# Optimization experiments

Measured on AMD Instinct MI355X. Metric: run time of the kernel, lower is better.

The kernel has to match this reference:

```python
import jax, jax.numpy as jnp
import numpy as np

N_ENT = 50000
N_REL = 16
D_E = 64
D_R = 64
D_OUT = 32
N_EDGE = 1000000


def setup_inputs() -> dict:
    key = jax.random.key(0)
    ks = jax.random.split(key, 8)
    # 0.1 scale keeps tanh / softmax in a realistic (non-saturated) range,
    # mimicking trained embedding magnitudes.
    entity_table = jax.random.normal(ks[0], (N_ENT, D_E), dtype=jnp.float32) * 0.1
    relation_table = jax.random.normal(ks[1], (N_REL, D_R), dtype=jnp.float32) * 0.1
    W_R = jax.random.normal(ks[2], (N_REL, D_E, D_R), dtype=jnp.float32) * (1.0 / np.sqrt(D_E))
    W1 = jax.random.normal(ks[3], (D_E, D_OUT), dtype=jnp.float32) * (1.0 / np.sqrt(D_E))
    b1 = jnp.zeros((D_OUT,), dtype=jnp.float32)
    W2 = jax.random.normal(ks[4], (D_E, D_OUT), dtype=jnp.float32) * (1.0 / np.sqrt(D_E))
    b2 = jnp.zeros((D_OUT,), dtype=jnp.float32)
    src = jax.random.randint(ks[5], (N_EDGE,), 0, N_ENT, dtype=jnp.int32)
    dst = jax.random.randint(ks[6], (N_EDGE,), 0, N_ENT, dtype=jnp.int32)
    etype = jax.random.randint(ks[7], (N_EDGE,), 0, N_REL, dtype=jnp.int32)
    return {"entity_table": entity_table, "relation_table": relation_table,
            "W_R": W_R, "W1": W1, "b1": b1, "W2": W2, "b2": b2,
            "src": src, "dst": dst, "etype": etype}


def reference(entity_table, relation_table, W_R, W1, b1, W2, b2, src, dst, etype):
    """KGAT calc_att (per-relation edge attention + edge softmax) followed by
    one bi-interaction Aggregator layer (dropout = identity, eval mode)."""
    n_nodes = entity_table.shape[0]
    # Per-relation projection of all node embeddings (grouped GEMM form of the
    # per-relation loop in compute_attention): [R, N, d_r]
    proj = jnp.einsum('nd,rde->rne', entity_table, W_R)
    r_mul_h = proj[etype, src]            # [E, d_r]  h W_r per edge
    r_mul_t = proj[etype, dst]            # [E, d_r]  t W_r per edge
    r_e = relation_table[etype]           # [E, d_r]
    # att = (h W_r) . tanh(t W_r + r)
    att = jnp.sum(r_mul_h * jnp.tanh(r_mul_t + r_e), axis=-1)  # [E]
    # edge softmax grouped by destination node
    att_max = jax.ops.segment_max(att, dst, num_segments=n_nodes)     # [N]
    ex = jnp.exp(att - att_max[dst])
    denom = jax.ops.segment_sum(ex, dst, num_segments=n_nodes)        # [N]
    a = ex / denom[dst]                                               # [E]
    # u_mul_e + sum: N_h[v] = sum_{(u->v)} a_e * node[u]
    msg = a[:, None] * entity_table[src]                              # [E, d]
    N_h = jax.ops.segment_sum(msg, dst, num_segments=n_nodes)         # [N, d]
    node = entity_table
    # bi-interaction aggregator (LeakyReLU slope 0.01, torch default)
    out1 = jax.nn.leaky_relu((node + N_h) @ W1 + b1)
    out2 = jax.nn.leaky_relu((node * N_h) @ W2 + b2)
    return out1 + out2
```

## Files before the change

kernel.cpp:

```cpp
#include <hip/hip_runtime.h>
#include <math.h>

#define NREL 16
#define DE 64
#define DOUT 32
#define NPART 16
#define TQ 392

typedef __attribute__((ext_vector_type(8))) short bf16x8;
typedef __attribute__((ext_vector_type(16))) float f32x16;
typedef __attribute__((ext_vector_type(2))) float f32x2;

__device__ __forceinline__ short f2bf(float f) {
    unsigned u = __builtin_bit_cast(unsigned, f);
    unsigned r = (u + 0x7FFFu + ((u >> 16) & 1u)) >> 16;
    return (short)r;
}
__device__ __forceinline__ float bf2f(short s) {
    unsigned u = ((unsigned)(unsigned short)s) << 16;
    return __builtin_bit_cast(float, u);
}
__device__ __forceinline__ unsigned char f2fp8(float f) {
    int p = __builtin_amdgcn_cvt_pk_fp8_f32(f, f, 0, false);
    return (unsigned char)(p & 0xff);
}
__device__ __forceinline__ unsigned cvt_pk_bf16(float lo, float hi) {
    unsigned r;
    asm("v_cvt_pk_bf16_f32 %0, %1, %2" : "=v"(r) : "v"(lo), "v"(hi));
    return r;
}
__device__ __forceinline__ float tanh_fast(float x) {
    float e = __expf(2.0f * x);
    return fmaf(-2.0f, __builtin_amdgcn_rcpf(e + 1.0f), 1.0f);
}

__global__ __launch_bounds__(256) void prep_kernel(const float* __restrict__ ent,
                                                   short* __restrict__ entbf,
                                                   unsigned char* __restrict__ entf8,
                                                   int eTot,
                                                   const float* __restrict__ WR,
                                                   short* __restrict__ WTbf,
                                                   const int* __restrict__ dst,
                                                   int* __restrict__ counts,
                                                   int E, int psz,
                                                   int eB, int wB) {
    int b = blockIdx.x;
    if (b < eB) {
        int i = b * 256 + threadIdx.x;
        if (i < eTot) {
            float f = ent[i];
            entbf[i] = f2bf(f);
            entf8[i] = f2fp8(f);
        }
    } else if (b < eB + wB) {
        int i = (b - eB) * 256 + threadIdx.x;
        int r = i >> 12, k = (i >> 6) & 63, j = i & 63;
        WTbf[(r << 12) + (j << 6) + k] = f2bf(WR[i]);
    } else {
        int hb = b - eB - wB;
        int part = hb & (NPART - 1);
        int i = (hb / NPART) * 256 + threadIdx.x;
        if (i < E) {
            int d = dst[i];
            if (d >= part * psz && d < (part + 1) * psz)
                atomicAdd(&counts[d], 1);
        }
    }
}

__global__ __launch_bounds__(256) void blocksum_kernel(const int* __restrict__ counts,
                                                       int* __restrict__ blockSums, int n) {
    __shared__ int wsum[4];
    int i = blockIdx.x * 256 + threadIdx.x;
    int v = (i < n) ? counts[i] : 0;
#pragma unroll
    for (int off = 1; off < 64; off <<= 1) v += __shfl_xor(v, off);
    if ((threadIdx.x & 63) == 0) wsum[threadIdx.x >> 6] = v;
    __syncthreads();
    if (threadIdx.x == 0)
        blockSums[blockIdx.x] = wsum[0] + wsum[1] + wsum[2] + wsum[3];
}

__global__ __launch_bounds__(1024) void blockscan_kernel(int* __restrict__ blockSums, int nb) {
    __shared__ int lds[1024];
    int t = threadIdx.x;
    int v = (t < nb) ? blockSums[t] : 0;
    lds[t] = v;
    __syncthreads();
    for (int off = 1; off < 1024; off <<= 1) {
        int u = (t >= off) ? lds[t - off] : 0;
        __syncthreads();
        lds[t] += u;
        __syncthreads();
    }
    if (t < nb) blockSums[t] = (t == 0) ? 0 : lds[t - 1];
}

__global__ __launch_bounds__(256) void scanout_kernel(const int* __restrict__ counts,
                                                      const int* __restrict__ blockSums,
                                                      int* __restrict__ offsets,
                                                      int* __restrict__ cursor, int n) {
    __shared__ int wsum[4];
    int t = threadIdx.x;
    int i = blockIdx.x * 256 + t;
    int lane = t & 63;
    int w = t >> 6;
    int v = (i < n) ? counts[i] : 0;
    int incl = v;
#pragma unroll
    for (int off = 1; off < 64; off <<= 1) {
        int u = __shfl_up(incl, off);
        if (lane >= off) incl += u;
    }
    if (lane == 63) wsum[w] = incl;
    __syncthreads();
    int woff = 0;
#pragma unroll
    for (int j = 0; j < 4; ++j) if (j < w) woff += wsum[j];
    int excl = incl - v + woff + blockSums[blockIdx.x];
    if (i < n) { offsets[i] = excl; cursor[i] = excl; }
    if (i == n - 1) offsets[n] = excl + v;
}

__global__ __launch_bounds__(256) void scatter_kernel(const int* __restrict__ dst,
                                                      const int* __restrict__ src,
                                                      const int* __restrict__ etype,
                                                      int* __restrict__ cursor,
                                                      int* __restrict__ pks,
                                                      int E, int psz) {
    int part = blockIdx.x & (NPART - 1);
    int i = (blockIdx.x / NPART) * 256 + threadIdx.x;
    if (i < E) {
        int d = dst[i];
        if (d >= part * psz && d < (part + 1) * psz) {
            int pos = atomicAdd(&cursor[d], 1);
            pks[pos] = (src[i] << 4) | etype[i];
        }
    }
}

__global__ __launch_bounds__(256) void projp_kernel(const short* __restrict__ entbf,
                                                    const short* __restrict__ WTbf,
                                                    unsigned char* __restrict__ Pf8,
                                                    int N) {
    __shared__ short Tl[4 * 1024];
    int lane = threadIdx.x & 63;
    int wid = threadIdx.x >> 6;
    int lin = blockIdx.x;
    int r = lin / TQ;
    int tq = lin - r * TQ;
    int m0 = (tq * 4 + wid) * 32;
    if (m0 >= N) return;
    int hi = lane >> 5;
    int lo = lane & 31;

    int arow = m0 + lo;
    if (arow >= N) arow = N - 1;
    const short* ap = entbf + ((size_t)arow << 6) + hi * 8;
    bf16x8 A[4];
#pragma unroll
    for (int kk = 0; kk < 4; ++kk) A[kk] = *(const bf16x8*)(ap + kk * 16);

    const short* wtb = WTbf + ((size_t)r << 12);

    f32x16 acc0 = {}, acc1 = {};
#pragma unroll
    for (int kk = 0; kk < 4; ++kk) {
        bf16x8 b0 = *(const bf16x8*)(wtb + lo * DE + kk * 16 + hi * 8);
        bf16x8 b1 = *(const bf16x8*)(wtb + (lo + 32) * DE + kk * 16 + hi * 8);
        acc0 = __builtin_amdgcn_mfma_f32_32x32x16_bf16(A[kk], b0, acc0, 0, 0, 0);
        acc1 = __builtin_amdgcn_mfma_f32_32x32x16_bf16(A[kk], b1, acc1, 0, 0, 0);
    }
    unsigned char* tb8 = (unsigned char*)(Tl + wid * 1024);
#pragma unroll
    for (int i = 0; i < 16; ++i) {
        int row = (i & 3) + 8 * (i >> 2) + 4 * hi;
        tb8[row * DE + lo] = f2fp8(acc0[i]);
        tb8[row * DE + 32 + lo] = f2fp8(acc1[i]);
    }
#pragma unroll
    for (int p = 0; p < 4; ++p) {
        int row = p * 8 + (lane >> 3);
        int node = m0 + row;
        unsigned long long vq = *(const unsigned long long*)(tb8 + row * DE + (lane & 7) * 8);
        if (node < N)
            __builtin_nontemporal_store(vq,
                (unsigned long long*)(Pf8 + (((size_t)r * N + node) << 6) + (lane & 7) * 8));
    }
}

__global__ __launch_bounds__(256) void agg_kernel(const float* __restrict__ ent,
                                                  const unsigned char* __restrict__ entf8,
                                                  const unsigned char* __restrict__ Pf8,
                                                  const float* __restrict__ rel,
                                                  const int* __restrict__ offsets,
                                                  const int* __restrict__ pks,
                                                  const float* __restrict__ W1,
                                                  const float* __restrict__ b1,
                                                  const float* __restrict__ W2,
                                                  const float* __restrict__ b2,
                                                  float* __restrict__ out, int n) {
    __shared__ float xl[4][128];
    __shared__ short tl[4][NREL * DE];
    int lane = threadIdx.x & 63;
    int wid = threadIdx.x >> 6;
    int v = (blockIdx.x << 2) + wid;
    if (v >= n) return;
    int o0 = offsets[v], o1 = offsets[v + 1];
    int g = lane >> 3, gl = lane & 7;

    short* tw = &tl[wid][0];
    const unsigned char* pv = Pf8 + ((size_t)v << 6);
#pragma unroll
    for (int pass = 0; pass < 4; ++pass) {
        int r = pass * 4 + (lane >> 4);
        int j4 = (lane & 15) * 4;
        unsigned pj = *(const unsigned*)(pv + (((size_t)r * (unsigned)n) << 6) + j4);
        f32x2 pa = __builtin_amdgcn_cvt_pk_f32_fp8(pj, false);
        f32x2 pb = __builtin_amdgcn_cvt_pk_f32_fp8(pj, true);
        float4 rv = *(const float4*)(rel + r * DE + j4);
        unsigned lo32 = cvt_pk_bf16(tanh_fast(pa[0] + rv.x), tanh_fast(pa[1] + rv.y));
        unsigned hi32 = cvt_pk_bf16(tanh_fast(pb[0] + rv.z), tanh_fast(pb[1] + rv.w));
        *(uint2*)(&tw[r * DE + j4]) = make_uint2(lo32, hi32);
    }

    float l = 0.f;
    float acc[8];
#pragma unroll
    for (int j = 0; j < 8; ++j) acc[j] = 0.f;

    int k0 = o0 + g;
    bool vv0 = k0 < o1;
    int pk0 = vv0 ? pks[k0] : 0;
    uint2 x0 = {}, h0 = {};
    if (vv0) {
        unsigned idx = (unsigned)(pk0 & 15) * (unsigned)n + (unsigned)(pk0 >> 4);
        x0 = *(const uint2*)(entf8 + ((size_t)(pk0 >> 4) << 6) + gl * 8);
        h0 = *(const uint2*)(Pf8 + ((size_t)idx << 6) + gl * 8);
    }
    int k1 = k0 + 8;
    bool vv1 = k1 < o1;
    int pk1 = vv1 ? pks[k1] : 0;
    uint2 x1 = {}, h1 = {};
    if (vv1) {
        unsigned idx = (unsigned)(pk1 & 15) * (unsigned)n + (unsigned)(pk1 >> 4);
        x1 = *(const uint2*)(entf8 + ((size_t)(pk1 >> 4) << 6) + gl * 8);
        h1 = *(const uint2*)(Pf8 + ((size_t)idx << 6) + gl * 8);
    }
    int k2 = k1 + 8;
    bool vv2 = k2 < o1;
    int pk2 = vv2 ? pks[k2] : 0;

    int iters = (o1 - o0 + 7) >> 3;
    for (int it = 0; it < iters; ++it) {
        uint2 x2 = {}, h2 = {};
        if (vv2) {
            unsigned idx = (unsigned)(pk2 & 15) * (unsigned)n + (unsigned)(pk2 >> 4);
            x2 = *(const uint2*)(entf8 + ((size_t)(pk2 >> 4) << 6) + gl * 8);
            h2 = *(const uint2*)(Pf8 + ((size_t)idx << 6) + gl * 8);
        }
        int k3 = k2 + 8;
        bool vv3 = k3 < o1;
        int pk3 = vv3 ? pks[k3] : 0;

        int rcur = pk0 & 15;
        bf16x8 tt = *(const bf16x8*)(&tw[(rcur << 6) + gl * 8]);
        f32x2 ha = __builtin_amdgcn_cvt_pk_f32_fp8(h0.x, false);
        f32x2 hb = __builtin_amdgcn_cvt_pk_f32_fp8(h0.x, true);
        f32x2 hc = __builtin_amdgcn_cvt_pk_f32_fp8(h0.y, false);
        f32x2 hd = __builtin_amdgcn_cvt_pk_f32_fp8(h0.y, true);
        f32x2 xa = __builtin_amdgcn_cvt_pk_f32_fp8(x0.x, false);
        f32x2 xb = __builtin_amdgcn_cvt_pk_f32_fp8(x0.x, true);
        f32x2 xc = __builtin_amdgcn_cvt_pk_f32_fp8(x0.y, false);
        f32x2 xd = __builtin_amdgcn_cvt_pk_f32_fp8(x0.y, true);
        float hf[8] = {ha[0], ha[1], hb[0], hb[1], hc[0], hc[1], hd[0], hd[1]};
        float xf[8] = {xa[0], xa[1], xb[0], xb[1], xc[0], xc[1], xd[0], xd[1]};
        float d = 0.f;
#pragma unroll
        for (int j = 0; j < 8; ++j)
            d = fmaf(hf[j], bf2f(tt[j]), d);
        d += __shfl_xor(d, 1);
        d += __shfl_xor(d, 2);
        d += __shfl_xor(d, 4);
        float pe = vv0 ? __expf(d) : 0.f;
        l += pe;
#pragma unroll
        for (int j = 0; j < 8; ++j) acc[j] = fmaf(pe, xf[j], acc[j]);
        vv0 = vv1; x0 = x1; h0 = h1; pk0 = pk1;
        vv1 = vv2; x1 = x2; h1 = h2; pk1 = pk2;
        vv2 = vv3; pk2 = pk3; k2 = k3;
    }
#pragma unroll
    for (int off = 8; off < 64; off <<= 1) {
        l += __shfl_xor(l, off);
#pragma unroll
        for (int j = 0; j < 8; ++j) acc[j] += __shfl_xor(acc[j], off);
    }
    float* xw = &xl[wid][0];
    float invl = (l > 0.f) ? (1.0f / l) : 0.f;
    if (g == 0) {
#pragma unroll
        for (int j = 0; j < 8; ++j) xw[gl * 8 + j] = acc[j] * invl;
    }
    float node = ent[((size_t)v << 6) + lane];
    float Nh = xw[lane];
    float x1e = node + Nh;
    float x2e = node * Nh;
    xw[lane] = x1e;
    xw[64 + lane] = x2e;
    int j = lane & 31;
    const float* __restrict__ Wsel = (lane < 32) ? W1 : W2;
    float bias = (lane < 32) ? b1[j] : b2[j];
    const float* xb2 = xw + ((lane < 32) ? 0 : 64);
    float o = 0.f;
#pragma unroll 8
    for (int kk = 0; kk < DE; ++kk)
        o = fmaf(xb2[kk], Wsel[kk * DOUT + j], o);
    o += bias;
    float lr = (o > 0.f) ? o : 0.01f * o;
    float other = __shfl_xor(lr, 32);
    if (lane < 32) out[(size_t)v * DOUT + lane] = lr + other;
}

extern "C" void kernel_launch(void* const* d_in, const int* in_sizes, int n_in,
                              void* d_out, int out_size, void* d_ws, size_t ws_size,
                              hipStream_t stream) {
    const float* ent = (const float*)d_in[0];
    const float* rel = (const float*)d_in[1];
    const float* WR  = (const float*)d_in[2];
    const float* W1  = (const float*)d_in[3];
    const float* b1  = (const float*)d_in[4];
    const float* W2  = (const float*)d_in[5];
    const float* b2  = (const float*)d_in[6];
    const int* src   = (const int*)d_in[7];
    const int* dst   = (const int*)d_in[8];
    const int* ety   = (const int*)d_in[9];
    float* out       = (float*)d_out;

    const int E = in_sizes[7];
    const int N = in_sizes[0] / DE;
    const int NB = (N + 255) / 256;
    const int psz = (N + NPART - 1) / NPART;
    const int chunks = (E + 255) / 256;

    size_t pBytes  = (size_t)N * NREL * DE;
    size_t eElems  = (size_t)N * DE;
    size_t wElems  = (size_t)NREL * DE * DE;

    char* ws = (char*)d_ws;
    unsigned char* Pf8 = (unsigned char*)ws;
    short* entbf = (short*)(ws + pBytes);
    short* WTbf  = entbf + eElems;
    unsigned char* entf8 = (unsigned char*)(WTbf + wElems);
    int* counts  = (int*)(entf8 + eElems);
    int* offsets = counts + N;
    int* cursor  = offsets + N + 1;
    int* pks     = cursor + N;
    int* bsums   = pks + E;
    size_t need  = (size_t)((char*)(bsums + NB) - ws);
    if (ws_size < need) return;

    const int eB = (int)((eElems + 255) / 256);
    const int wB = (int)(wElems / 256);

    hipMemsetAsync(counts, 0, (size_t)N * 4, stream);
    prep_kernel<<<eB + wB + chunks * NPART, 256, 0, stream>>>(
        ent, entbf, entf8, (int)eElems, WR, WTbf, dst, counts, E, psz, eB, wB);
    blocksum_kernel<<<NB, 256, 0, stream>>>(counts, bsums, N);
    blockscan_kernel<<<1, 1024, 0, stream>>>(bsums, NB);
    scanout_kernel<<<NB, 256, 0, stream>>>(counts, bsums, offsets, cursor, N);
    scatter_kernel<<<chunks * NPART, 256, 0, stream>>>(dst, src, ety, cursor, pks, E, psz);
    projp_kernel<<<TQ * NREL, 256, 0, stream>>>(entbf, WTbf, Pf8, N);
    agg_kernel<<<(N + 3) / 4, 256, 0, stream>>>(ent, entf8, Pf8, rel, offsets, pks,
                                                W1, b1, W2, b2, out, N);
}
```

Before: 220.6 us.

## Widen agg gathers to 16-byte loads, store tanh table in fp8, remap blocks

In the aggregation kernel, each edge is now handled by 4 lanes with 16-byte fp8 loads instead of 8 lanes with 8-byte loads, so twice as many edges are processed per iteration. The per-relation tanh table in shared memory is stored as fp8 instead of bf16, which halves LDS traffic per edge. A block-index remap groups blocks so that neighbouring vertices are spread across the 8 XCDs in contiguous runs. The projection output store is also changed from nontemporal to a normal store so the results stay in cache for the later gathers. In exchange, the fp8 tanh values lose precision and the wider per-lane accumulators raise register pressure.

New measurement: 240.4 us. +9.0%, slower.

```diff
diff --git a/kernel.cpp b/kernel.cpp
--- a/kernel.cpp
+++ b/kernel.cpp
@@ -16,22 +16,27 @@
     unsigned r = (u + 0x7FFFu + ((u >> 16) & 1u)) >> 16;
     return (short)r;
 }
-__device__ __forceinline__ float bf2f(short s) {
-    unsigned u = ((unsigned)(unsigned short)s) << 16;
-    return __builtin_bit_cast(float, u);
-}
 __device__ __forceinline__ unsigned char f2fp8(float f) {
     int p = __builtin_amdgcn_cvt_pk_fp8_f32(f, f, 0, false);
     return (unsigned char)(p & 0xff);
 }
-__device__ __forceinline__ unsigned cvt_pk_bf16(float lo, float hi) {
-    unsigned r;
-    asm("v_cvt_pk_bf16_f32 %0, %1, %2" : "=v"(r) : "v"(lo), "v"(hi));
-    return r;
-}
 __device__ __forceinline__ float tanh_fast(float x) {
     float e = __expf(2.0f * x);
     return fmaf(-2.0f, __builtin_amdgcn_rcpf(e + 1.0f), 1.0f);
+}
+__device__ __forceinline__ void fp8x16_to_f32(uint4 u, float* f) {
+    f32x2 a0 = __builtin_amdgcn_cvt_pk_f32_fp8(u.x, false);
+    f32x2 a1 = __builtin_amdgcn_cvt_pk_f32_fp8(u.x, true);
+    f32x2 a2 = __builtin_amdgcn_cvt_pk_f32_fp8(u.y, false);
+    f32x2 a3 = __builtin_amdgcn_cvt_pk_f32_fp8(u.y, true);
+    f32x2 a4 = __builtin_amdgcn_cvt_pk_f32_fp8(u.z, false);
+    f32x2 a5 = __builtin_amdgcn_cvt_pk_f32_fp8(u.z, true);
+    f32x2 a6 = __builtin_amdgcn_cvt_pk_f32_fp8(u.w, false);
+    f32x2 a7 = __builtin_amdgcn_cvt_pk_f32_fp8(u.w, true);
+    f[0] = a0[0]; f[1] = a0[1]; f[2] = a1[0]; f[3] = a1[1];
+    f[4] = a2[0]; f[5] = a2[1]; f[6] = a3[0]; f[7] = a3[1];
+    f[8] = a4[0]; f[9] = a4[1]; f[10] = a5[0]; f[11] = a5[1];
+    f[12] = a6[0]; f[13] = a6[1]; f[14] = a7[0]; f[15] = a7[1];
 }
 
 __global__ __launch_bounds__(256) void prep_kernel(const float* __restrict__ ent,
@@ -184,8 +189,7 @@
         int node = m0 + row;
         unsigned long long vq = *(const unsigned long long*)(tb8 + row * DE + (lane & 7) * 8);
         if (node < N)
-            __builtin_nontemporal_store(vq,
-                (unsigned long long*)(Pf8 + (((size_t)r * N + node) << 6) + (lane & 7) * 8));
+            *(unsigned long long*)(Pf8 + (((size_t)r * N + node) << 6) + (lane & 7) * 8) = vq;
     }
 }
 
@@ -199,17 +203,24 @@
                                                   const float* __restrict__ b1,
                                                   const float* __restrict__ W2,
                                                   const float* __restrict__ b2,
-                                                  float* __restrict__ out, int n) {
+                                                  float* __restrict__ out,
+                                                  int n, int nb) {
     __shared__ float xl[4][128];
-    __shared__ short tl[4][NREL * DE];
+    __shared__ unsigned char tl[4][NREL * DE];
+    {
+    }
+    int x8 = blockIdx.x & 7;
+    int rank = blockIdx.x >> 3;
+    int orig = (rank >> 5) * 256 + x8 * 32 + (rank & 31);
+    if (orig >= nb) return;
     int lane = threadIdx.x & 63;
     int wid = threadIdx.x >> 6;
-    int v = (blockIdx.x << 2) + wid;
+    int v = (orig << 2) + wid;
     if (v >= n) return;
     int o0 = offsets[v], o1 = offsets[v + 1];
-    int g = lane >> 3, gl = lane & 7;
-
-    short* tw = &tl[wid][0];
+    int g = lane >> 2, gl = lane & 3;
+
+    unsigned char* tw = &tl[wid][0];
     const unsigned char* pv = Pf8 + ((size_t)v << 6);
 #pragma unroll
     for (int pass = 0; pass < 4; ++pass) {
@@ -219,88 +230,82 @@
         f32x2 pa = __builtin_amdgcn_cvt_pk_f32_fp8(pj, false);
         f32x2 pb = __builtin_amdgcn_cvt_pk_f32_fp8(pj, true);
         float4 rv = *(const float4*)(rel + r * DE + j4);
-        unsigned lo32 = cvt_pk_bf16(tanh_fast(pa[0] + rv.x), tanh_fast(pa[1] + rv.y));
-        unsigned hi32 = cvt_pk_bf16(tanh_fast(pb[0] + rv.z), tanh_fast(pb[1] + rv.w));
-        *(uint2*)(&tw[r * DE + j4]) = make_uint2(lo32, hi32);
+        float t0 = tanh_fast(pa[0] + rv.x), t1 = tanh_fast(pa[1] + rv.y);
+        float t2 = tanh_fast(pb[0] + rv.z), t3 = tanh_fast(pb[1] + rv.w);
+        int p01 = __builtin_amdgcn_cvt_pk_fp8_f32(t0, t1, 0, false);
+        int p03 = __builtin_amdgcn_cvt_pk_fp8_f32(t2, t3, p01, true);
+        *(int*)(&tw[(r << 6) + j4]) = p03;
     }
 
     float l = 0.f;
-    float acc[8];
-#pragma unroll
-    for (int j = 0; j < 8; ++j) acc[j] = 0.f;
+    float acc[16];
+#pragma unroll
+    for (int j = 0; j < 16; ++j) acc[j] = 0.f;
 
     int k0 = o0 + g;
     bool vv0 = k0 < o1;
     int pk0 = vv0 ? pks[k0] : 0;
-    uint2 x0 = {}, h0 = {};
+    uint4 x0 = {}, h0 = {};
     if (vv0) {
         unsigned idx = (unsigned)(pk0 & 15) * (unsigned)n + (unsigned)(pk0 >> 4);
-        x0 = *(const uint2*)(entf8 + ((size_t)(pk0 >> 4) << 6) + gl * 8);
-        h0 = *(const uint2*)(Pf8 + ((size_t)idx << 6) + gl * 8);
-    }
-    int k1 = k0 + 8;
+        x0 = *(const uint4*)(entf8 + ((size_t)(pk0 >> 4) << 6) + gl * 16);
+        h0 = *(const uint4*)(Pf8 + ((size_t)idx << 6) + gl * 16);
+    }
+    int k1 = k0 + 16;
     bool vv1 = k1 < o1;
     int pk1 = vv1 ? pks[k1] : 0;
-    uint2 x1 = {}, h1 = {};
+    uint4 x1 = {}, h1 = {};
     if (vv1) {
         unsigned idx = (unsigned)(pk1 & 15) * (unsigned)n + (unsigned)(pk1 >> 4);
-        x1 = *(const uint2*)(entf8 + ((size_t)(pk1 >> 4) << 6) + gl * 8);
-        h1 = *(const uint2*)(Pf8 + ((size_t)idx << 6) + gl * 8);
-    }
-    int k2 = k1 + 8;
+        x1 = *(const uint4*)(entf8 + ((size_t)(pk1 >> 4) << 6) + gl * 16);
+        h1 = *(const uint4*)(Pf8 + ((size_t)idx << 6) + gl * 16);
+    }
+    int k2 = k1 + 16;
     bool vv2 = k2 < o1;
     int pk2 = vv2 ? pks[k2] : 0;
 
-    int iters = (o1 - o0 + 7) >> 3;
+    int iters = (o1 - o0 + 15) >> 4;
     for (int it = 0; it < iters; ++it) {
-        uint2 x2 = {}, h2 = {};
+        uint4 x2 = {}, h2 = {};
         if (vv2) {
             unsigned idx = (unsigned)(pk2 & 15) * (unsigned)n + (unsigned)(pk2 >> 4);
-            x2 = *(const uint2*)(entf8 + ((size_t)(pk2 >> 4) << 6) + gl * 8);
-            h2 = *(const uint2*)(Pf8 + ((size_t)idx << 6) + gl * 8);
+            x2 = *(const uint4*)(entf8 + ((size_t)(pk2 >> 4) << 6) + gl * 16);
+            h2 = *(const uint4*)(Pf8 + ((size_t)idx << 6) + gl * 16);
         }
-        int k3 = k2 + 8;
+        int k3 = k2 + 16;
         bool vv3 = k3 < o1;
         int pk3 = vv3 ? pks[k3] : 0;
 
         int rcur = pk0 & 15;
-        bf16x8 tt = *(const bf16x8*)(&tw[(rcur << 6) + gl * 8]);
-        f32x2 ha = __builtin_amdgcn_cvt_pk_f32_fp8(h0.x, false);
-        f32x2 hb = __builtin_amdgcn_cvt_pk_f32_fp8(h0.x, true);
-        f32x2 hc = __builtin_amdgcn_cvt_pk_f32_fp8(h0.y, false);
-        f32x2 hd = __builtin_amdgcn_cvt_pk_f32_fp8(h0.y, true);
-        f32x2 xa = __builtin_amdgcn_cvt_pk_f32_fp8(x0.x, false);
-        f32x2 xb = __builtin_amdgcn_cvt_pk_f32_fp8(x0.x, true);
-        f32x2 xc = __builtin_amdgcn_cvt_pk_f32_fp8(x0.y, false);
-        f32x2 xd = __builtin_amdgcn_cvt_pk_f32_fp8(x0.y, true);
-        float hf[8] = {ha[0], ha[1], hb[0], hb[1], hc[0], hc[1], hd[0], hd[1]};
-        float xf[8] = {xa[0], xa[1], xb[0], xb[1], xc[0], xc[1], xd[0], xd[1]};
+        uint4 tt = *(const uint4*)(&tw[(rcur << 6) + gl * 16]);
+        float hf[16], xf[16], tf[16];
+        fp8x16_to_f32(h0, hf);
+        fp8x16_to_f32(x0, xf);
+        fp8x16_to_f32(tt, tf);
         float d = 0.f;
 #pragma unroll
-        for (int j = 0; j < 8; ++j)
-            d = fmaf(hf[j], bf2f(tt[j]), d);
+        for (int j = 0; j < 16; ++j) d = fmaf(hf[j], tf[j], d);
         d += __shfl_xor(d, 1);
         d += __shfl_xor(d, 2);
-        d += __shfl_xor(d, 4);
         float pe = vv0 ? __expf(d) : 0.f;
         l += pe;
 #pragma unroll
-        for (int j = 0; j < 8; ++j) acc[j] = fmaf(pe, xf[j], acc[j]);
+        for (int j = 0; j < 16; ++j) acc[j] = fmaf(pe, xf[j], acc[j]);
         vv0 = vv1; x0 = x1; h0 = h1; pk0 = pk1;
         vv1 = vv2; x1 = x2; h1 = h2; pk1 = pk2;
         vv2 = vv3; pk2 = pk3; k2 = k3;
     }
 #pragma unroll
-    for (int off = 8; off < 64; off <<= 1) {
+    for (int off = 4; off < 64; off <<= 1) {
         l += __shfl_xor(l, off);
 #pragma unroll
-        for (int j = 0; j < 8; ++j) acc[j] += __shfl_xor(acc[j], off);
+        for (int j = 0; j < 16; ++j) acc[j] += __shfl_xor(acc[j], off);
     }
     float* xw = &xl[wid][0];
     float invl = (l > 0.f) ? (1.0f / l) : 0.f;
     if (g == 0) {
 #pragma unroll
-        for (int j = 0; j < 8; ++j) xw[gl * 8 + j] = acc[j] * invl;
+        for (int j = 0; j < 16; ++j) xw[gl * 16 + j] = acc[j] * invl;
     }
     float node = ent[((size_t)v << 6) + lane];
     float Nh = xw[lane];
@@ -362,6 +367,8 @@
 
     const int eB = (int)((eElems + 255) / 256);
     const int wB = (int)(wElems / 256);
+    const int nbAgg = (N + 3) / 4;
+    const int gridAgg = ((nbAgg + 255) / 256) * 256;
 
     hipMemsetAsync(counts, 0, (size_t)N * 4, stream);
     prep_kernel<<<eB + wB + chunks * NPART, 256, 0, stream>>>(
@@ -371,6 +378,6 @@
     scanout_kernel<<<NB, 256, 0, stream>>>(counts, bsums, offsets, cursor, N);
     scatter_kernel<<<chunks * NPART, 256, 0, stream>>>(dst, src, ety, cursor, pks, E, psz);
     projp_kernel<<<TQ * NREL, 256, 0, stream>>>(entbf, WTbf, Pf8, N);
-    agg_kernel<<<(N + 3) / 4, 256, 0, stream>>>(ent, entf8, Pf8, rel, offsets, pks,
-                                                W1, b1, W2, b2, out, N);
-}
+    agg_kernel<<<gridAgg, 256, 0, stream>>>(ent, entf8, Pf8, rel, offsets, pks,
+                                            W1, b1, W2, b2, out, N, nbAgg);
+}
```

## Precompute per-destination Q = W_r·tanh(tW_r+r) so edges gather only source rows

Applied to the files above, without the earlier changes.

Rewrites the attention as h·W_r·tanh(tW_r+r) = x_src · (W_r tanh(tW_r+r)), computing Q[r,v] once per (relation,node) in the projection kernel with a second MFMA GEMM. The aggregation kernel then loads only Q for the destination node and the source entity fp8 row, dropping the per-edge gather of the projected source row from the 16-relation table. The projection kernel does more work (tanh plus a second GEMM through swizzled LDS), and the reassociation adds rounding through bf16 and fp8 intermediates.

After: 227.9 us. +3.3%, slower.

```diff
diff --git a/kernel.cpp b/kernel.cpp
--- a/kernel.cpp
+++ b/kernel.cpp
@@ -16,22 +16,21 @@
     unsigned r = (u + 0x7FFFu + ((u >> 16) & 1u)) >> 16;
     return (short)r;
 }
-__device__ __forceinline__ float bf2f(short s) {
-    unsigned u = ((unsigned)(unsigned short)s) << 16;
-    return __builtin_bit_cast(float, u);
-}
 __device__ __forceinline__ unsigned char f2fp8(float f) {
     int p = __builtin_amdgcn_cvt_pk_fp8_f32(f, f, 0, false);
     return (unsigned char)(p & 0xff);
 }
-__device__ __forceinline__ unsigned cvt_pk_bf16(float lo, float hi) {
-    unsigned r;
-    asm("v_cvt_pk_bf16_f32 %0, %1, %2" : "=v"(r) : "v"(lo), "v"(hi));
-    return r;
-}
 __device__ __forceinline__ float tanh_fast(float x) {
     float e = __expf(2.0f * x);
     return fmaf(-2.0f, __builtin_amdgcn_rcpf(e + 1.0f), 1.0f);
+}
+__device__ __forceinline__ void fp8x8_to_f32(uint2 u, float* f) {
+    f32x2 a0 = __builtin_amdgcn_cvt_pk_f32_fp8(u.x, false);
+    f32x2 a1 = __builtin_amdgcn_cvt_pk_f32_fp8(u.x, true);
+    f32x2 a2 = __builtin_amdgcn_cvt_pk_f32_fp8(u.y, false);
+    f32x2 a3 = __builtin_amdgcn_cvt_pk_f32_fp8(u.y, true);
+    f[0] = a0[0]; f[1] = a0[1]; f[2] = a1[0]; f[3] = a1[1];
+    f[4] = a2[0]; f[5] = a2[1]; f[6] = a3[0]; f[7] = a3[1];
 }
 
 __global__ __launch_bounds__(256) void prep_kernel(const float* __restrict__ ent,
@@ -39,6 +38,7 @@
                                                    unsigned char* __restrict__ entf8,
                                                    int eTot,
                                                    const float* __restrict__ WR,
+                                                   short* __restrict__ Wbf,
                                                    short* __restrict__ WTbf,
                                                    const int* __restrict__ dst,
                                                    int* __restrict__ counts,
@@ -55,7 +55,9 @@
     } else if (b < eB + wB) {
         int i = (b - eB) * 256 + threadIdx.x;
         int r = i >> 12, k = (i >> 6) & 63, j = i & 63;
-        WTbf[(r << 12) + (j << 6) + k] = f2bf(WR[i]);
+        short w = f2bf(WR[i]);
+        Wbf[i] = w;
+        WTbf[(r << 12) + (j << 6) + k] = w;
     } else {
         int hb = b - eB - wB;
         int part = hb & (NPART - 1);
@@ -139,11 +141,13 @@
     }
 }
 
-__global__ __launch_bounds__(256) void projp_kernel(const short* __restrict__ entbf,
+__global__ __launch_bounds__(256) void projq_kernel(const short* __restrict__ entbf,
+                                                    const float* __restrict__ rel,
+                                                    const short* __restrict__ Wbf,
                                                     const short* __restrict__ WTbf,
-                                                    unsigned char* __restrict__ Pf8,
+                                                    unsigned char* __restrict__ Qf8,
                                                     int N) {
-    __shared__ short Tl[4 * 1024];
+    __shared__ short Tl[4 * 2048];
     int lane = threadIdx.x & 63;
     int wid = threadIdx.x >> 6;
     int lin = blockIdx.x;
@@ -161,7 +165,9 @@
 #pragma unroll
     for (int kk = 0; kk < 4; ++kk) A[kk] = *(const bf16x8*)(ap + kk * 16);
 
+    short* tb = Tl + wid * 2048;
     const short* wtb = WTbf + ((size_t)r << 12);
+    const short* wb  = Wbf  + ((size_t)r << 12);
 
     f32x16 acc0 = {}, acc1 = {};
 #pragma unroll
@@ -171,12 +177,34 @@
         acc0 = __builtin_amdgcn_mfma_f32_32x32x16_bf16(A[kk], b0, acc0, 0, 0, 0);
         acc1 = __builtin_amdgcn_mfma_f32_32x32x16_bf16(A[kk], b1, acc1, 0, 0, 0);
     }
-    unsigned char* tb8 = (unsigned char*)(Tl + wid * 1024);
+    float rv0 = rel[r * DE + lo];
+    float rv1 = rel[r * DE + 32 + lo];
 #pragma unroll
     for (int i = 0; i < 16; ++i) {
         int row = (i & 3) + 8 * (i >> 2) + 4 * hi;
-        tb8[row * DE + lo] = f2fp8(acc0[i]);
-        tb8[row * DE + 32 + lo] = f2fp8(acc1[i]);
+        int sw = (row & 7) << 3;
+        tb[(row * DE + lo) ^ sw] = f2bf(tanh_fast(acc0[i] + rv0));
+        tb[(row * DE + 32 + lo) ^ sw] = f2bf(tanh_fast(acc1[i] + rv1));
+    }
+    bf16x8 A2[4];
+#pragma unroll
+    for (int kk = 0; kk < 4; ++kk)
+        A2[kk] = *(const bf16x8*)(tb + ((lo * DE + kk * 16 + hi * 8) ^ ((lo & 7) << 3)));
+
+    f32x16 q0 = {}, q1 = {};
+#pragma unroll
+    for (int kk = 0; kk < 4; ++kk) {
+        bf16x8 b0 = *(const bf16x8*)(wb + lo * DE + kk * 16 + hi * 8);
+        bf16x8 b1 = *(const bf16x8*)(wb + (lo + 32) * DE + kk * 16 + hi * 8);
+        q0 = __builtin_amdgcn_mfma_f32_32x32x16_bf16(A2[kk], b0, q0, 0, 0, 0);
+        q1 = __builtin_amdgcn_mfma_f32_32x32x16_bf16(A2[kk], b1, q1, 0, 0, 0);
+    }
+    unsigned char* tb8 = (unsigned char*)tb;
+#pragma unroll
+    for (int i = 0; i < 16; ++i) {
+        int row = (i & 3) + 8 * (i >> 2) + 4 * hi;
+        tb8[row * DE + lo] = f2fp8(q0[i]);
+        tb8[row * DE + 32 + lo] = f2fp8(q1[i]);
     }
 #pragma unroll
     for (int p = 0; p < 4; ++p) {
@@ -184,15 +212,13 @@
         int node = m0 + row;
         unsigned long long vq = *(const unsigned long long*)(tb8 + row * DE + (lane & 7) * 8);
         if (node < N)
-            __builtin_nontemporal_store(vq,
-                (unsigned long long*)(Pf8 + (((size_t)r * N + node) << 6) + (lane & 7) * 8));
+            *(unsigned long long*)(Qf8 + (((size_t)r * N + node) << 6) + (lane & 7) * 8) = vq;
     }
 }
 
 __global__ __launch_bounds__(256) void agg_kernel(const float* __restrict__ ent,
                                                   const unsigned char* __restrict__ entf8,
-                                                  const unsigned char* __restrict__ Pf8,
-                                                  const float* __restrict__ rel,
+                                                  const unsigned char* __restrict__ Qf8,
                                                   const int* __restrict__ offsets,
                                                   const int* __restrict__ pks,
                                                   const float* __restrict__ W1,
@@ -201,7 +227,7 @@
                                                   const float* __restrict__ b2,
                                                   float* __restrict__ out, int n) {
     __shared__ float xl[4][128];
-    __shared__ short tl[4][NREL * DE];
+    __shared__ unsigned char ql[4][NREL * DE];
     int lane = threadIdx.x & 63;
     int wid = threadIdx.x >> 6;
     int v = (blockIdx.x << 2) + wid;
@@ -209,19 +235,13 @@
     int o0 = offsets[v], o1 = offsets[v + 1];
     int g = lane >> 3, gl = lane & 7;
 
-    short* tw = &tl[wid][0];
-    const unsigned char* pv = Pf8 + ((size_t)v << 6);
+    unsigned char* qw = &ql[wid][0];
 #pragma unroll
     for (int pass = 0; pass < 4; ++pass) {
         int r = pass * 4 + (lane >> 4);
         int j4 = (lane & 15) * 4;
-        unsigned pj = *(const unsigned*)(pv + (((size_t)r * (unsigned)n) << 6) + j4);
-        f32x2 pa = __builtin_amdgcn_cvt_pk_f32_fp8(pj, false);
-        f32x2 pb = __builtin_amdgcn_cvt_pk_f32_fp8(pj, true);
-        float4 rv = *(const float4*)(rel + r * DE + j4);
-        unsigned lo32 = cvt_pk_bf16(tanh_fast(pa[0] + rv.x), tanh_fast(pa[1] + rv.y));
-        unsigned hi32 = cvt_pk_bf16(tanh_fast(pb[0] + rv.z), tanh_fast(pb[1] + rv.w));
-        *(uint2*)(&tw[r * DE + j4]) = make_uint2(lo32, hi32);
+        unsigned qj = *(const unsigned*)(Qf8 + (((size_t)r * (unsigned)n + (unsigned)v) << 6) + j4);
+        *(unsigned*)(&qw[(r << 6) + j4]) = qj;
     }
 
     float l = 0.f;
@@ -232,53 +252,33 @@
     int k0 = o0 + g;
     bool vv0 = k0 < o1;
     int pk0 = vv0 ? pks[k0] : 0;
-    uint2 x0 = {}, h0 = {};
-    if (vv0) {
-        unsigned idx = (unsigned)(pk0 & 15) * (unsigned)n + (unsigned)(pk0 >> 4);
-        x0 = *(const uint2*)(entf8 + ((size_t)(pk0 >> 4) << 6) + gl * 8);
-        h0 = *(const uint2*)(Pf8 + ((size_t)idx << 6) + gl * 8);
-    }
+    uint2 x0 = {};
+    if (vv0) x0 = *(const uint2*)(entf8 + ((size_t)(pk0 >> 4) << 6) + gl * 8);
     int k1 = k0 + 8;
     bool vv1 = k1 < o1;
     int pk1 = vv1 ? pks[k1] : 0;
-    uint2 x1 = {}, h1 = {};
-    if (vv1) {
-        unsigned idx = (unsigned)(pk1 & 15) * (unsigned)n + (unsigned)(pk1 >> 4);
-        x1 = *(const uint2*)(entf8 + ((size_t)(pk1 >> 4) << 6) + gl * 8);
-        h1 = *(const uint2*)(Pf8 + ((size_t)idx << 6) + gl * 8);
-    }
+    uint2 x1 = {};
+    if (vv1) x1 = *(const uint2*)(entf8 + ((size_t)(pk1 >> 4) << 6) + gl * 8);
     int k2 = k1 + 8;
     bool vv2 = k2 < o1;
     int pk2 = vv2 ? pks[k2] : 0;
 
     int iters = (o1 - o0 + 7) >> 3;
     for (int it = 0; it < iters; ++it) {
-        uint2 x2 = {}, h2 = {};
-        if (vv2) {
-            unsigned idx = (unsigned)(pk2 & 15) * (unsigned)n + (unsigned)(pk2 >> 4);
-            x2 = *(const uint2*)(entf8 + ((size_t)(pk2 >> 4) << 6) + gl * 8);
-            h2 = *(const uint2*)(Pf8 + ((size_t)idx << 6) + gl * 8);
-        }
+        uint2 x2 = {};
+        if (vv2) x2 = *(const uint2*)(entf8 + ((size_t)(pk2 >> 4) << 6) + gl * 8);
         int k3 = k2 + 8;
         bool vv3 = k3 < o1;
         int pk3 = vv3 ? pks[k3] : 0;
 
         int rcur = pk0 & 15;
-        bf16x8 tt = *(const bf16x8*)(&tw[(rcur << 6) + gl * 8]);
-        f32x2 ha = __builtin_amdgcn_cvt_pk_f32_fp8(h0.x, false);
-        f32x2 hb = __builtin_amdgcn_cvt_pk_f32_fp8(h0.x, true);
-        f32x2 hc = __builtin_amdgcn_cvt_pk_f32_fp8(h0.y, false);
-        f32x2 hd = __builtin_amdgcn_cvt_pk_f32_fp8(h0.y, true);
-        f32x2 xa = __builtin_amdgcn_cvt_pk_f32_fp8(x0.x, false);
-        f32x2 xb = __builtin_amdgcn_cvt_pk_f32_fp8(x0.x, true);
-        f32x2 xc = __builtin_amdgcn_cvt_pk_f32_fp8(x0.y, false);
-        f32x2 xd = __builtin_amdgcn_cvt_pk_f32_fp8(x0.y, true);
-        float hf[8] = {ha[0], ha[1], hb[0], hb[1], hc[0], hc[1], hd[0], hd[1]};
-        float xf[8] = {xa[0], xa[1], xb[0], xb[1], xc[0], xc[1], xd[0], xd[1]};
+        uint2 qv = *(const uint2*)(&qw[(rcur << 6) + gl * 8]);
+        float xf[8], qf[8];
+        fp8x8_to_f32(x0, xf);
+        fp8x8_to_f32(qv, qf);
         float d = 0.f;
 #pragma unroll
-        for (int j = 0; j < 8; ++j)
-            d = fmaf(hf[j], bf2f(tt[j]), d);
+        for (int j = 0; j < 8; ++j) d = fmaf(xf[j], qf[j], d);
         d += __shfl_xor(d, 1);
         d += __shfl_xor(d, 2);
         d += __shfl_xor(d, 4);
@@ -286,8 +286,8 @@
         l += pe;
 #pragma unroll
         for (int j = 0; j < 8; ++j) acc[j] = fmaf(pe, xf[j], acc[j]);
-        vv0 = vv1; x0 = x1; h0 = h1; pk0 = pk1;
-        vv1 = vv2; x1 = x2; h1 = h2; pk1 = pk2;
+        vv0 = vv1; x0 = x1; pk0 = pk1;
+        vv1 = vv2; x1 = x2; pk1 = pk2;
         vv2 = vv3; pk2 = pk3; k2 = k3;
     }
 #pragma unroll
@@ -343,14 +343,15 @@
     const int psz = (N + NPART - 1) / NPART;
     const int chunks = (E + 255) / 256;
 
-    size_t pBytes  = (size_t)N * NREL * DE;
+    size_t qBytes  = (size_t)N * NREL * DE;
     size_t eElems  = (size_t)N * DE;
     size_t wElems  = (size_t)NREL * DE * DE;
 
     char* ws = (char*)d_ws;
-    unsigned char* Pf8 = (unsigned char*)ws;
-    short* entbf = (short*)(ws + pBytes);
-    short* WTbf  = entbf + eElems;
+    unsigned char* Qf8 = (unsigned char*)ws;
+    short* entbf = (short*)(ws + qBytes);
+    short* Wbf   = entbf + eElems;
+    short* WTbf  = Wbf + wElems;
     unsigned char* entf8 = (unsigned char*)(WTbf + wElems);
     int* counts  = (int*)(entf8 + eElems);
     int* offsets = counts + N;
@@ -365,12 +366,12 @@
 
     hipMemsetAsync(counts, 0, (size_t)N * 4, stream);
     prep_kernel<<<eB + wB + chunks * NPART, 256, 0, stream>>>(
-        ent, entbf, entf8, (int)eElems, WR, WTbf, dst, counts, E, psz, eB, wB);
+        ent, entbf, entf8, (int)eElems, WR, Wbf, WTbf, dst, counts, E, psz, eB, wB);
     blocksum_kernel<<<NB, 256, 0, stream>>>(counts, bsums, N);
     blockscan_kernel<<<1, 1024, 0, stream>>>(bsums, NB);
     scanout_kernel<<<NB, 256, 0, stream>>>(counts, bsums, offsets, cursor, N);
     scatter_kernel<<<chunks * NPART, 256, 0, stream>>>(dst, src, ety, cursor, pks, E, psz);
-    projp_kernel<<<TQ * NREL, 256, 0, stream>>>(entbf, WTbf, Pf8, N);
-    agg_kernel<<<(N + 3) / 4, 256, 0, stream>>>(ent, entf8, Pf8, rel, offsets, pks,
+    projq_kernel<<<TQ * NREL, 256, 0, stream>>>(entbf, rel, Wbf, WTbf, Qf8, N);
+    agg_kernel<<<(N + 3) / 4, 256, 0, stream>>>(ent, entf8, Qf8, offsets, pks,
                                                 W1, b1, W2, b2, out, N);
 }
```
